# Kernel optimization log

Hardware: AMD Instinct MI355X
Metric: run time of the kernel (lower is better)

The kernel has to match this reference:

```python
import jax, jax.numpy as jnp
import numpy as np

B, N, K, C = 8, 4096, 32, 128
HEAD_DIM = 64          # out_channels(512) // num_heads(8)
POS_DIM = HEAD_DIM // 2
D_THRESHOLD = 0.04


def setup_inputs() -> dict:
    key = jax.random.key(0)
    ks = jax.random.split(key, 16)

    def W(k, fi, fo):
        return (jax.random.normal(k, (fi, fo), jnp.float32) / np.sqrt(fi)).astype(jnp.float32)

    return {
        "center_xyz": jax.random.normal(ks[0], (B, N, 3), jnp.float32),
        "center_features": jax.random.normal(ks[1], (B, N, C), jnp.float32),
        "neighbor_xyz": jax.random.normal(ks[2], (B, N, K, 3), jnp.float32),
        "neighbor_features": jax.random.normal(ks[3], (B, N, K, C), jnp.float32),
        "phi_w": W(ks[4], C, HEAD_DIM),   "phi_b": jnp.zeros((HEAD_DIM,), jnp.float32),
        "theta_w": W(ks[5], C, HEAD_DIM), "theta_b": jnp.zeros((HEAD_DIM,), jnp.float32),
        "m1_w": W(ks[6], 3, POS_DIM),     "m1_b": jnp.zeros((POS_DIM,), jnp.float32),
        "m2_w": W(ks[7], 3, POS_DIM),     "m2_b": jnp.zeros((POS_DIM,), jnp.float32),
        "psi_w": W(ks[8], 2 * POS_DIM, 1), "psi_b": jnp.zeros((1,), jnp.float32),
        "z_w": W(ks[9], C, HEAD_DIM),     "z_b": jnp.zeros((HEAD_DIM,), jnp.float32),
    }


def reference(center_xyz, center_features, neighbor_xyz, neighbor_features,
              phi_w, phi_b, theta_w, theta_b, m1_w, m1_b, m2_w, m2_b,
              psi_w, psi_b, z_w, z_b):
    relu = jax.nn.relu
    # feature affinity r_f: (B,N,K,1)
    feat_i = relu(center_features @ phi_w + phi_b)        # (B,N,H)
    feat_j = relu(neighbor_features @ theta_w + theta_b)  # (B,N,K,H)
    r_f = jnp.sum(feat_i[:, :, None, :] * feat_j, axis=-1, keepdims=True)
    # positional score r_l_base: (B,N,K,1)
    pos_i = relu(center_xyz @ m1_w + m1_b)                # (B,N,P)
    pos_j = relu(neighbor_xyz @ m2_w + m2_b)              # (B,N,K,P)
    pos_i_t = jnp.broadcast_to(pos_i[:, :, None, :], pos_j.shape)
    r_l_base = relu(jnp.concatenate([pos_i_t, pos_j], axis=-1) @ psi_w + psi_b)
    # SPIL mask: same frame (z coord equal) AND distance > threshold
    t_i = center_xyz[..., 2][:, :, None]                  # (B,N,1)
    t_j = neighbor_xyz[..., 2]                            # (B,N,K)
    same_frame = (t_i == t_j).astype(jnp.float32)
    euclid = jnp.linalg.norm(center_xyz[:, :, None, :] - neighbor_xyz, axis=-1)
    dist_mask = (euclid > D_THRESHOLD).astype(jnp.float32)
    mask = same_frame * dist_mask                         # (B,N,K)
    r_l = r_l_base * (1.0 - mask[..., None])
    # masked, r_l-weighted softmax over K
    r_f = r_f / jnp.sqrt(jnp.float32(HEAD_DIM))
    r_f_max = jnp.max(r_f, axis=2, keepdims=True)
    numerator = r_l * jnp.exp(r_f - r_f_max)
    denominator = jnp.sum(numerator, axis=2, keepdims=True) + 1e-8
    W_ij = numerator / denominator                        # (B,N,K,1)
    transformed = neighbor_features @ z_w + z_b           # (B,N,K,H)
    return jnp.sum(W_ij * transformed, axis=2)            # (B,N,H)
```

## Files before the change

kernel.cpp:

```cpp
#include <hip/hip_runtime.h>
#include <hip/hip_bf16.h>


#define Bq 8
#define Nq 4096
#define Kq 32
#define Cq 128
#define Hq 64

typedef __bf16 bf16x8 __attribute__((ext_vector_type(8)));
typedef float  f32x4  __attribute__((ext_vector_type(4)));

__device__ __forceinline__ unsigned short f2bf(float f) {
  __hip_bfloat16 h = __float2bfloat16(f);
  return *reinterpret_cast<unsigned short*>(&h);
}
__device__ __forceinline__ float bf2f(unsigned short u) {
  return __uint_as_float(((unsigned int)u) << 16);
}

__global__ __launch_bounds__(256) void prep_w(const float* __restrict__ theta_w,
                                              const float* __restrict__ z_w,
                                              unsigned short* __restrict__ WcT) {
  int idx = blockIdx.x * 256 + threadIdx.x;
  int h = idx >> 7, c = idx & 127;
  float v = (h < 64) ? theta_w[c * 64 + h] : z_w[c * 64 + (h - 64)];
  WcT[idx] = f2bf(v);
}

__global__ __launch_bounds__(256) void prep_feat(
    const float* __restrict__ cf, const float* __restrict__ cxyz,
    const float* __restrict__ phi_w, const float* __restrict__ phi_b,
    const float* __restrict__ m1_w, const float* __restrict__ m1_b,
    const float* __restrict__ psi_w,
    float* __restrict__ feat_out, float* __restrict__ s_out) {
  __shared__ float phi_s[128 * 64];
  __shared__ float cf_s[8 * 128];
  const int t = threadIdx.x;
  const size_t n0 = (size_t)blockIdx.x * 8;
  for (int i = t; i < 128 * 64; i += 256) phi_s[i] = phi_w[i];
  for (int i = t; i < 8 * 128; i += 256) cf_s[i] = cf[n0 * 128 + i];
  __syncthreads();
  const int h = t & 63;
  const int rg = t >> 6;
  float a0 = phi_b[h], a1 = a0;
  const float* r0 = &cf_s[(2 * rg) * 128];
  const float* r1 = &cf_s[(2 * rg + 1) * 128];
  for (int c = 0; c < 128; c++) {
    float w = phi_s[c * 64 + h];
    a0 = fmaf(r0[c], w, a0);
    a1 = fmaf(r1[c], w, a1);
  }
  feat_out[(n0 + 2 * rg) * 64 + h]     = fmaxf(a0, 0.f);
  feat_out[(n0 + 2 * rg + 1) * 64 + h] = fmaxf(a1, 0.f);
  if (t < 8) {
    size_t n = n0 + t;
    float x = cxyz[n * 3], y = cxyz[n * 3 + 1], z = cxyz[n * 3 + 2];
    float s = 0.f;
    for (int p = 0; p < 32; p++) {
      float pi = fmaxf(x * m1_w[p] + y * m1_w[32 + p] + z * m1_w[64 + p] + m1_b[p], 0.f);
      s += pi * psi_w[p];
    }
    s_out[n] = s;
  }
}

__global__ __launch_bounds__(256, 2) void spil_main(
    const float* __restrict__ cxyz, const float* __restrict__ nxyz,
    const float* __restrict__ nf,
    const float* __restrict__ theta_b, const float* __restrict__ m2_w,
    const float* __restrict__ m2_b, const float* __restrict__ psi_w,
    const float* __restrict__ psi_b, const float* __restrict__ z_b,
    const unsigned short* __restrict__ WcT,
    const float* __restrict__ feat_i, const float* __restrict__ s_i,
    float* __restrict__ out) {
  __shared__ __align__(16) char smem[65536];
  unsigned short* Xs   = (unsigned short*)smem;
  unsigned short* Ws   = (unsigned short*)(smem + 32768);
  unsigned short* outt = (unsigned short*)smem;
  float* feat_s = (float*)(smem + 33792);
  float* m2w_s  = feat_s + 256;
  float* m2b_s  = m2w_s + 96;
  float* psij_s = m2b_s + 32;
  float* zb_s   = psij_s + 32;
  float* tb_s   = zb_s + 64;

  const int t = threadIdx.x;
  const int wave = t >> 6, lane = t & 63;
  const int lo16 = lane & 15, quad = lane >> 4;
  const size_t n0 = (size_t)blockIdx.x * 4;

  const float4* xsrc = (const float4*)(nf + n0 * Kq * Cq);
  ushort4* xdst = (ushort4*)Xs;
#pragma unroll
  for (int i = 0; i < 16; i++) {
    float4 v = xsrc[t + i * 256];
    ushort4 p;
    p.x = f2bf(v.x); p.y = f2bf(v.y); p.z = f2bf(v.z); p.w = f2bf(v.w);
    xdst[t + i * 256] = p;
  }
  const uint4* wsrc = (const uint4*)WcT;
  uint4* wdst = (uint4*)Ws;
#pragma unroll
  for (int i = 0; i < 8; i++) wdst[t + i * 256] = wsrc[t + i * 256];
  __syncthreads();

  const int mhalf = wave & 1, nhalf = wave >> 1;
  const bf16x8* Xv = (const bf16x8*)Xs;
  const bf16x8* Wv = (const bf16x8*)Ws;
  f32x4 acc[4][4];
#pragma unroll
  for (int mt = 0; mt < 4; mt++)
#pragma unroll
    for (int nt = 0; nt < 4; nt++) acc[mt][nt] = (f32x4){0.f, 0.f, 0.f, 0.f};
#pragma unroll
  for (int ks = 0; ks < 4; ks++) {
    bf16x8 a[4], b[4];
#pragma unroll
    for (int mt = 0; mt < 4; mt++)
      a[mt] = Xv[(mhalf * 64 + mt * 16 + lo16) * 16 + ks * 4 + quad];
#pragma unroll
    for (int nt = 0; nt < 4; nt++)
      b[nt] = Wv[(nhalf * 64 + nt * 16 + lo16) * 16 + ks * 4 + quad];
#pragma unroll
    for (int mt = 0; mt < 4; mt++)
#pragma unroll
      for (int nt = 0; nt < 4; nt++)
        acc[mt][nt] = __builtin_amdgcn_mfma_f32_16x16x32_bf16(a[mt], b[nt], acc[mt][nt], 0, 0, 0);
  }
  __syncthreads();

#pragma unroll
  for (int mt = 0; mt < 4; mt++) {
    int row0 = mhalf * 64 + mt * 16 + quad * 4;
#pragma unroll
    for (int nt = 0; nt < 4; nt++) {
      int col = nhalf * 64 + nt * 16 + lo16;
#pragma unroll
      for (int r = 0; r < 4; r++)
        outt[(row0 + r) * 132 + col] = f2bf(acc[mt][nt][r]);
    }
  }
  feat_s[t] = feat_i[n0 * 64 + t];
  if (t < 96) m2w_s[t] = m2_w[t];
  if (t < 32) { m2b_s[t] = m2_b[t]; psij_s[t] = psi_w[32 + t]; }
  if (t < 64) { zb_s[t] = z_b[t]; tb_s[t] = theta_b[t]; }
  __syncthreads();

  const int nl = wave;
  const size_t ng = n0 + nl;
  const int k = lane & 31, half = lane >> 5;
  const int baser = nl * 32;

  const float* fi = feat_s + nl * 64;
  const unsigned short* orow = outt + (size_t)(baser + k) * 132;
  float v = 0.f;
#pragma unroll
  for (int i = 0; i < 32; i++) {
    int h = half * 32 + i;
    float fj = fmaxf(bf2f(orow[h]) + tb_s[h], 0.f);
    v = fmaf(fj, fi[h], v);
  }
  v += __shfl_xor(v, 32);
  float r_f = v * 0.125f;

  float cx = cxyz[ng * 3 + 0], cy = cxyz[ng * 3 + 1], cz = cxyz[ng * 3 + 2];
  const float* nxp = nxyz + (ng * Kq + (size_t)k) * 3;
  float xj = nxp[0], yj = nxp[1], zj = nxp[2];
  float sj = 0.f;
#pragma unroll
  for (int p = 0; p < 32; p++) {
    float pj = fmaxf(fmaf(xj, m2w_s[p], fmaf(yj, m2w_s[32 + p], fmaf(zj, m2w_s[64 + p], m2b_s[p]))), 0.f);
    sj = fmaf(pj, psij_s[p], sj);
  }
  float rl = fmaxf(s_i[ng] + sj + psi_b[0], 0.f);
  float dx = cx - xj, dy = cy - yj, dz = cz - zj;
  float dist = sqrtf(dx * dx + dy * dy + dz * dz);
  if (cz == zj && dist > 0.04f) rl = 0.f;

  float m = r_f;
#pragma unroll
  for (int off = 16; off; off >>= 1) m = fmaxf(m, __shfl_xor(m, off));
  float e = rl * __expf(r_f - m);
  float s = e;
#pragma unroll
  for (int off = 16; off; off >>= 1) s += __shfl_xor(s, off);
  float wgt = e / (s + 1e-8f);

  const int h = lane;
  const float zb = zb_s[h];
  float o = 0.f;
#pragma unroll
  for (int kk = 0; kk < 32; kk++) {
    float w = __shfl(wgt, kk);
    o = fmaf(w, bf2f(outt[(baser + kk) * 132 + 64 + h]) + zb, o);
  }
  out[ng * 64 + h] = o;
}

extern "C" void kernel_launch(void* const* d_in, const int* in_sizes, int n_in,
                              void* d_out, int out_size, void* d_ws, size_t ws_size,
                              hipStream_t stream) {
  const float* cxyz    = (const float*)d_in[0];
  const float* cf      = (const float*)d_in[1];
  const float* nxyz    = (const float*)d_in[2];
  const float* nf      = (const float*)d_in[3];
  const float* phi_w   = (const float*)d_in[4];
  const float* phi_b   = (const float*)d_in[5];
  const float* theta_w = (const float*)d_in[6];
  const float* theta_b = (const float*)d_in[7];
  const float* m1_w    = (const float*)d_in[8];
  const float* m1_b    = (const float*)d_in[9];
  const float* m2_w    = (const float*)d_in[10];
  const float* m2_b    = (const float*)d_in[11];
  const float* psi_w   = (const float*)d_in[12];
  const float* psi_b   = (const float*)d_in[13];
  const float* z_w     = (const float*)d_in[14];
  const float* z_b     = (const float*)d_in[15];
  float* outp = (float*)d_out;

  char* ws = (char*)d_ws;
  unsigned short* WcT = (unsigned short*)ws;
  float* feat = (float*)(ws + 32768);
  float* s_i  = (float*)(ws + 32768 + (size_t)Bq * Nq * 64 * 4);

  prep_w<<<64, 256, 0, stream>>>(theta_w, z_w, WcT);
  prep_feat<<<(Bq * Nq) / 8, 256, 0, stream>>>(cf, cxyz, phi_w, phi_b, m1_w, m1_b, psi_w, feat, s_i);
  spil_main<<<(Bq * Nq) / 4, 256, 0, stream>>>(cxyz, nxyz, nf, theta_b, m2_w, m2_b, psi_w, psi_b,
                                               z_b, WcT, feat, s_i, outp);
}
```

Measured before the change: 803.9 us.

## Use MFMA for phi projection, keep weights in registers, swizzle LDS tiles

Replaces the scalar FP32 phi projection kernel with a bf16 MFMA GEMM that handles 128 center points per block, using a pre-transposed bf16 phi weight. In the main kernel, the theta/z weight fragments are loaded straight from global memory into registers instead of being staged in LDS. This frees 32KB of LDS and allows the occupancy hint to rise from 2 to 3 blocks. The neighbor feature tile in LDS is now XOR-swizzled to avoid bank conflicts on MFMA operand reads. The cost is more register pressure from the 16 held weight fragments, and the phi projection now runs at bf16 precision.

```diff
diff --git a/kernel.cpp b/kernel.cpp
--- a/kernel.cpp
+++ b/kernel.cpp
@@ -21,51 +21,103 @@
 
 __global__ __launch_bounds__(256) void prep_w(const float* __restrict__ theta_w,
                                               const float* __restrict__ z_w,
-                                              unsigned short* __restrict__ WcT) {
+                                              const float* __restrict__ phi_w,
+                                              unsigned short* __restrict__ WcT,
+                                              unsigned short* __restrict__ phiT) {
   int idx = blockIdx.x * 256 + threadIdx.x;
-  int h = idx >> 7, c = idx & 127;
-  float v = (h < 64) ? theta_w[c * 64 + h] : z_w[c * 64 + (h - 64)];
-  WcT[idx] = f2bf(v);
-}
-
-__global__ __launch_bounds__(256) void prep_feat(
+  if (idx < 16384) {
+    int h = idx >> 7, c = idx & 127;
+    float v = (h < 64) ? theta_w[c * 64 + h] : z_w[c * 64 + (h - 64)];
+    WcT[idx] = f2bf(v);
+  } else {
+    int i2 = idx - 16384;
+    int h = i2 >> 7, c = i2 & 127;
+    phiT[i2] = f2bf(phi_w[c * 64 + h]);
+  }
+}
+
+__global__ __launch_bounds__(256) void phi_gemm(
     const float* __restrict__ cf, const float* __restrict__ cxyz,
-    const float* __restrict__ phi_w, const float* __restrict__ phi_b,
+    const unsigned short* __restrict__ phiT, const float* __restrict__ phi_b,
     const float* __restrict__ m1_w, const float* __restrict__ m1_b,
     const float* __restrict__ psi_w,
     float* __restrict__ feat_out, float* __restrict__ s_out) {
-  __shared__ float phi_s[128 * 64];
-  __shared__ float cf_s[8 * 128];
+  __shared__ __align__(16) unsigned short Xs[128 * 128];
   const int t = threadIdx.x;
-  const size_t n0 = (size_t)blockIdx.x * 8;
-  for (int i = t; i < 128 * 64; i += 256) phi_s[i] = phi_w[i];
-  for (int i = t; i < 8 * 128; i += 256) cf_s[i] = cf[n0 * 128 + i];
-  __syncthreads();
-  const int h = t & 63;
-  const int rg = t >> 6;
-  float a0 = phi_b[h], a1 = a0;
-  const float* r0 = &cf_s[(2 * rg) * 128];
-  const float* r1 = &cf_s[(2 * rg + 1) * 128];
-  for (int c = 0; c < 128; c++) {
-    float w = phi_s[c * 64 + h];
-    a0 = fmaf(r0[c], w, a0);
-    a1 = fmaf(r1[c], w, a1);
-  }
-  feat_out[(n0 + 2 * rg) * 64 + h]     = fmaxf(a0, 0.f);
-  feat_out[(n0 + 2 * rg + 1) * 64 + h] = fmaxf(a1, 0.f);
-  if (t < 8) {
+  const int wave = t >> 6, lane = t & 63;
+  const int lo16 = lane & 15, quad = lane >> 4;
+  const size_t n0 = (size_t)blockIdx.x * 128;
+
+  bf16x8 wf[4][4];
+#pragma unroll
+  for (int ks = 0; ks < 4; ks++)
+#pragma unroll
+    for (int nt = 0; nt < 4; nt++)
+      wf[ks][nt] = *(const bf16x8*)(phiT + (size_t)(nt * 16 + lo16) * 128 + ks * 32 + quad * 8);
+
+  const float4* xsrc = (const float4*)(cf + n0 * Cq);
+  ushort4* xdst4 = (ushort4*)Xs;
+#pragma unroll
+  for (int i = 0; i < 16; i++) {
+    int j = t + i * 256;
+    float4 v = xsrc[j];
+    int r = j >> 5, w = j & 31;
+    int g = w >> 1, hf = w & 1;
+    int p = g ^ (r & 15);
+    ushort4 pk;
+    pk.x = f2bf(v.x); pk.y = f2bf(v.y); pk.z = f2bf(v.z); pk.w = f2bf(v.w);
+    xdst4[r * 32 + p * 2 + hf] = pk;
+  }
+  __syncthreads();
+
+  f32x4 acc[2][4];
+#pragma unroll
+  for (int mt = 0; mt < 2; mt++)
+#pragma unroll
+    for (int nt = 0; nt < 4; nt++) acc[mt][nt] = (f32x4){0.f, 0.f, 0.f, 0.f};
+#pragma unroll
+  for (int ks = 0; ks < 4; ks++) {
+    int p = (ks * 4 + quad) ^ lo16;
+    bf16x8 a[2];
+#pragma unroll
+    for (int mt = 0; mt < 2; mt++) {
+      int row = wave * 32 + mt * 16 + lo16;
+      a[mt] = *(const bf16x8*)(Xs + row * 128 + p * 8);
+    }
+#pragma unroll
+    for (int mt = 0; mt < 2; mt++)
+#pragma unroll
+      for (int nt = 0; nt < 4; nt++)
+        acc[mt][nt] = __builtin_amdgcn_mfma_f32_16x16x32_bf16(a[mt], wf[ks][nt], acc[mt][nt], 0, 0, 0);
+  }
+
+#pragma unroll
+  for (int mt = 0; mt < 2; mt++)
+#pragma unroll
+    for (int nt = 0; nt < 4; nt++) {
+      int h = nt * 16 + lo16;
+      float b = phi_b[h];
+#pragma unroll
+      for (int r = 0; r < 4; r++) {
+        int row = wave * 32 + mt * 16 + quad * 4 + r;
+        feat_out[(n0 + row) * 64 + h] = fmaxf(acc[mt][nt][r] + b, 0.f);
+      }
+    }
+
+  if (t < 128) {
     size_t n = n0 + t;
     float x = cxyz[n * 3], y = cxyz[n * 3 + 1], z = cxyz[n * 3 + 2];
     float s = 0.f;
+#pragma unroll 4
     for (int p = 0; p < 32; p++) {
-      float pi = fmaxf(x * m1_w[p] + y * m1_w[32 + p] + z * m1_w[64 + p] + m1_b[p], 0.f);
-      s += pi * psi_w[p];
+      float pi = fmaxf(fmaf(x, m1_w[p], fmaf(y, m1_w[32 + p], fmaf(z, m1_w[64 + p], m1_b[p]))), 0.f);
+      s = fmaf(pi, psi_w[p], s);
     }
     s_out[n] = s;
   }
 }
 
-__global__ __launch_bounds__(256, 2) void spil_main(
+__global__ __launch_bounds__(256, 3) void spil_main(
     const float* __restrict__ cxyz, const float* __restrict__ nxyz,
     const float* __restrict__ nf,
     const float* __restrict__ theta_b, const float* __restrict__ m2_w,
@@ -74,9 +126,8 @@
     const unsigned short* __restrict__ WcT,
     const float* __restrict__ feat_i, const float* __restrict__ s_i,
     float* __restrict__ out) {
-  __shared__ __align__(16) char smem[65536];
+  __shared__ __align__(16) char smem[35968];
   unsigned short* Xs   = (unsigned short*)smem;
-  unsigned short* Ws   = (unsigned short*)(smem + 32768);
   unsigned short* outt = (unsigned short*)smem;
   float* feat_s = (float*)(smem + 33792);
   float* m2w_s  = feat_s + 256;
@@ -90,24 +141,29 @@
   const int lo16 = lane & 15, quad = lane >> 4;
   const size_t n0 = (size_t)blockIdx.x * 4;
 
+  const int mhalf = wave & 1, nhalf = wave >> 1;
+  bf16x8 wf[4][4];
+#pragma unroll
+  for (int ks = 0; ks < 4; ks++)
+#pragma unroll
+    for (int nt = 0; nt < 4; nt++)
+      wf[ks][nt] = *(const bf16x8*)(WcT + (size_t)(nhalf * 64 + nt * 16 + lo16) * 128 + ks * 32 + quad * 8);
+
   const float4* xsrc = (const float4*)(nf + n0 * Kq * Cq);
-  ushort4* xdst = (ushort4*)Xs;
+  ushort4* xdst4 = (ushort4*)Xs;
 #pragma unroll
   for (int i = 0; i < 16; i++) {
-    float4 v = xsrc[t + i * 256];
-    ushort4 p;
-    p.x = f2bf(v.x); p.y = f2bf(v.y); p.z = f2bf(v.z); p.w = f2bf(v.w);
-    xdst[t + i * 256] = p;
-  }
-  const uint4* wsrc = (const uint4*)WcT;
-  uint4* wdst = (uint4*)Ws;
-#pragma unroll
-  for (int i = 0; i < 8; i++) wdst[t + i * 256] = wsrc[t + i * 256];
-  __syncthreads();
-
-  const int mhalf = wave & 1, nhalf = wave >> 1;
-  const bf16x8* Xv = (const bf16x8*)Xs;
-  const bf16x8* Wv = (const bf16x8*)Ws;
+    int j = t + i * 256;
+    float4 v = xsrc[j];
+    int r = j >> 5, w = j & 31;
+    int g = w >> 1, hf = w & 1;
+    int p = g ^ (r & 15);
+    ushort4 pk;
+    pk.x = f2bf(v.x); pk.y = f2bf(v.y); pk.z = f2bf(v.z); pk.w = f2bf(v.w);
+    xdst4[r * 32 + p * 2 + hf] = pk;
+  }
+  __syncthreads();
+
   f32x4 acc[4][4];
 #pragma unroll
   for (int mt = 0; mt < 4; mt++)
@@ -115,18 +171,18 @@
     for (int nt = 0; nt < 4; nt++) acc[mt][nt] = (f32x4){0.f, 0.f, 0.f, 0.f};
 #pragma unroll
   for (int ks = 0; ks < 4; ks++) {
-    bf16x8 a[4], b[4];
+    int p = (ks * 4 + quad) ^ lo16;
+    bf16x8 a[4];
+#pragma unroll
+    for (int mt = 0; mt < 4; mt++) {
+      int row = mhalf * 64 + mt * 16 + lo16;
+      a[mt] = *(const bf16x8*)(Xs + row * 128 + p * 8);
+    }
 #pragma unroll
     for (int mt = 0; mt < 4; mt++)
-      a[mt] = Xv[(mhalf * 64 + mt * 16 + lo16) * 16 + ks * 4 + quad];
-#pragma unroll
-    for (int nt = 0; nt < 4; nt++)
-      b[nt] = Wv[(nhalf * 64 + nt * 16 + lo16) * 16 + ks * 4 + quad];
-#pragma unroll
-    for (int mt = 0; mt < 4; mt++)
 #pragma unroll
       for (int nt = 0; nt < 4; nt++)
-        acc[mt][nt] = __builtin_amdgcn_mfma_f32_16x16x32_bf16(a[mt], b[nt], acc[mt][nt], 0, 0, 0);
+        acc[mt][nt] = __builtin_amdgcn_mfma_f32_16x16x32_bf16(a[mt], wf[ks][nt], acc[mt][nt], 0, 0, 0);
   }
   __syncthreads();
 
@@ -220,12 +276,13 @@
   float* outp = (float*)d_out;
 
   char* ws = (char*)d_ws;
-  unsigned short* WcT = (unsigned short*)ws;
-  float* feat = (float*)(ws + 32768);
-  float* s_i  = (float*)(ws + 32768 + (size_t)Bq * Nq * 64 * 4);
-
-  prep_w<<<64, 256, 0, stream>>>(theta_w, z_w, WcT);
-  prep_feat<<<(Bq * Nq) / 8, 256, 0, stream>>>(cf, cxyz, phi_w, phi_b, m1_w, m1_b, psi_w, feat, s_i);
+  unsigned short* WcT  = (unsigned short*)ws;
+  unsigned short* phiT = (unsigned short*)(ws + 32768);
+  float* feat = (float*)(ws + 49152);
+  float* s_i  = (float*)(ws + 49152 + (size_t)Bq * Nq * 64 * 4);
+
+  prep_w<<<96, 256, 0, stream>>>(theta_w, z_w, phi_w, WcT, phiT);
+  phi_gemm<<<(Bq * Nq) / 128, 256, 0, stream>>>(cf, cxyz, phiT, phi_b, m1_w, m1_b, psi_w, feat, s_i);
   spil_main<<<(Bq * Nq) / 4, 256, 0, stream>>>(cxyz, nxyz, nf, theta_b, m2_w, m2_b, psi_w, psi_b,
                                                z_b, WcT, feat, s_i, outp);
 }
```

Result: faster. 746.9 us (-7.1%).
